# Performance work log

Hardware: AMD Instinct MI355X
Metric: run time of the kernel (lower is better)

The kernel has to match this reference:

```python
import jax, jax.numpy as jnp
import numpy as np

N_NODES = 100000
N_EDGES = 1600000
D_IN, D_HID, N_CLS = 256, 128, 47


def setup_inputs() -> dict:
    key = jax.random.key(0)
    k = jax.random.split(key, 5)
    x = jax.random.normal(k[0], (N_NODES, D_IN), dtype=jnp.float32)
    edge_index = jax.random.randint(k[1], (2, N_EDGES), 0, N_NODES, dtype=jnp.int64)
    W1 = jax.random.normal(k[2], (D_IN, D_HID), dtype=jnp.float32) * 0.05
    b1 = jnp.zeros((D_HID,), dtype=jnp.float32)
    W2 = jax.random.normal(k[3], (D_HID, N_CLS), dtype=jnp.float32) * 0.05
    b2 = jnp.zeros((N_CLS,), dtype=jnp.float32)
    return {"x": x, "edge_index": edge_index, "W1": W1, "b1": b1, "W2": W2, "b2": b2}


def _gcn_conv(x, W, b, src, dst, norm, n):
    # PyG GCNConv: linear transform, normalized scatter-add aggregation, bias after
    h = x @ W                                   # [N, D_out]
    msg = h[src] * norm[:, None]                # gather over edges [E', D_out]
    agg = jax.ops.segment_sum(msg, dst, num_segments=n)
    return agg + b


def reference(x, edge_index, W1, b1, W2, b2):
    n = x.shape[0]
    loop = jnp.arange(n, dtype=edge_index.dtype)
    src = jnp.concatenate([edge_index[0], loop])  # add self-loops
    dst = jnp.concatenate([edge_index[1], loop])
    # symmetric normalization D^-1/2 (A+I) D^-1/2 (degree = in-degree incl. self-loop)
    deg = jax.ops.segment_sum(jnp.ones_like(dst, dtype=x.dtype), dst, num_segments=n)
    dinv = jnp.where(deg > 0, jax.lax.rsqrt(deg), 0.0)
    norm = dinv[src] * dinv[dst]                 # [E']
    h1 = jax.nn.relu(_gcn_conv(x, W1, b1, src, dst, norm, n))
    # dropout with training=False is identity
    out = _gcn_conv(h1, W2, b2, src, dst, norm, n)
    return out
```

## Files before the change

### kernel.cpp

```cpp
#include <hip/hip_runtime.h>
#include <hip/hip_bf16.h>

#define DIN 256
#define DHID 128
#define NCLS 47
#define BSHIFT 9
#define BNODES 512
#define NPART 1024
#define BCAPS 9216
#define CHUNKE 1600

typedef __attribute__((ext_vector_type(8))) short short8;
typedef __attribute__((ext_vector_type(4))) float f32x4;

__device__ __forceinline__ short f2bf(float f) {
    __bf16 b = (__bf16)f;
    return __builtin_bit_cast(short, b);
}
__device__ __forceinline__ float bfu(unsigned int u) {
    return __uint_as_float(u << 16);
}
__device__ __forceinline__ float bfh(unsigned int u) {
    return __uint_as_float(u & 0xffff0000u);
}
__device__ __forceinline__ unsigned int pack2(float lo, float hi) {
    return (unsigned int)(unsigned short)f2bf(lo)
         | ((unsigned int)(unsigned short)f2bf(hi) << 16);
}
__device__ __forceinline__ void add8(float* a, uint4 v) {
    a[0] += bfu(v.x); a[1] += bfh(v.x);
    a[2] += bfu(v.y); a[3] += bfh(v.y);
    a[4] += bfu(v.z); a[5] += bfh(v.z);
    a[6] += bfu(v.w); a[7] += bfh(v.w);
}
__device__ __forceinline__ void fma8(float* a, uint4 v, float d) {
    a[0] += d * bfu(v.x); a[1] += d * bfh(v.x);
    a[2] += d * bfu(v.y); a[3] += d * bfh(v.y);
    a[4] += d * bfu(v.z); a[5] += d * bfh(v.z);
    a[6] += d * bfu(v.w); a[7] += d * bfh(v.w);
}

__global__ __launch_bounds__(256) void k_prep_hist(const float* __restrict__ W1,
                                                   const float* __restrict__ W2,
                                                   short* __restrict__ W1s,
                                                   short* __restrict__ W2s,
                                                   const int* __restrict__ dst,
                                                   int* __restrict__ ghist,
                                                   int E, int NB, int chunk) {
    __shared__ int lh[256];
    int blk = blockIdx.x, t = threadIdx.x;
    if (blk < 16) {
        int tid = blk * 256 + t;
        int frag = tid >> 6, lane = tid & 63;
        int kt = frag >> 3, nt = frag & 7;
        int quad = lane >> 4, col = lane & 15;
        #pragma unroll
        for (int j = 0; j < 8; ++j) {
            int k = kt * 32 + quad * 8 + j;
            W1s[(size_t)tid * 8 + j] = f2bf(W1[k * DHID + nt * 16 + col]);
        }
    } else if (blk < 20) {
        int tid = (blk - 16) * 256 + t;
        int frag = tid >> 6, lane = tid & 63;
        int kt = frag >> 2, nt = frag & 3;
        int quad = lane >> 4, col = lane & 15;
        int c = nt * 16 + col;
        #pragma unroll
        for (int j = 0; j < 8; ++j) {
            int k = kt * 32 + quad * 8 + j;
            float v = (c < NCLS) ? W2[k * NCLS + c] : 0.0f;
            W2s[(size_t)tid * 8 + j] = f2bf(v);
        }
    } else {
        int p = blk - 20;
        for (int i = t; i < NB; i += 256) lh[i] = 0;
        __syncthreads();
        int lo = p * chunk, hi = min(E, lo + chunk);
        for (int i = lo + t; i < hi; i += 256)
            atomicAdd(&lh[dst[i] >> BSHIFT], 1);
        __syncthreads();
        for (int i = t; i < NB; i += 256) ghist[(size_t)i * NPART + p] = lh[i];
    }
}

__global__ __launch_bounds__(256) void k_colscan(const int* __restrict__ ghist,
                                                 int* __restrict__ goff,
                                                 int* __restrict__ btot) {
    __shared__ int wsum[4];
    int b = blockIdx.x, t = threadIdx.x;
    int4 v = ((const int4*)(ghist + (size_t)b * NPART))[t];
    int s = v.x + v.y + v.z + v.w;
    int incl = s;
    int lane = t & 63, w = t >> 6;
    #pragma unroll
    for (int off = 1; off < 64; off <<= 1) {
        int u = __shfl_up(incl, off, 64);
        if (lane >= off) incl += u;
    }
    if (lane == 63) wsum[w] = incl;
    __syncthreads();
    int wadd = 0;
    for (int i = 0; i < w; ++i) wadd += wsum[i];
    int ex = wadd + incl - s;
    int4 o;
    o.x = ex; o.y = ex + v.x; o.z = o.y + v.y; o.w = o.z + v.z;
    ((int4*)(goff + (size_t)b * NPART))[t] = o;
    if (t == 255) btot[b] = wadd + incl;
}

__device__ __forceinline__ void scan_btot(const int* __restrict__ btot, int NB,
                                          int* lbase, int* wsum) {
    int t = threadIdx.x;
    int v = (t < NB) ? btot[t] : 0;
    int incl = v;
    int lane = t & 63, w = t >> 6;
    #pragma unroll
    for (int off = 1; off < 64; off <<= 1) {
        int u = __shfl_up(incl, off, 64);
        if (lane >= off) incl += u;
    }
    if (lane == 63) wsum[w] = incl;
    __syncthreads();
    int wadd = 0;
    for (int i = 0; i < w; ++i) wadd += wsum[i];
    lbase[t] = wadd + incl - v;
    __syncthreads();
}

__global__ __launch_bounds__(256) void k_scatter_gemm1(const int* __restrict__ src,
                                                       const int* __restrict__ dst,
                                                       const int* __restrict__ ghist,
                                                       const int* __restrict__ goff,
                                                       const int* __restrict__ btot,
                                                       unsigned int* __restrict__ bbuf,
                                                       int E, int NB, int chunk,
                                                       const float* __restrict__ x,
                                                       const short* __restrict__ W1s,
                                                       short* __restrict__ hb, int n) {
    __shared__ unsigned int stage[CHUNKE];
    __shared__ int sdest[CHUNKE];
    __shared__ int lcur[256];
    __shared__ int gdst[256];
    __shared__ int wsum[4];

    int blk = blockIdx.x, t = threadIdx.x;

    if (blk < NPART) {
        int p = blk;
        scan_btot(btot, NB, gdst, wsum);

        int mine = (t < NB) ? ghist[(size_t)t * NPART + p] : 0;
        int incl = mine;
        int lane = t & 63, w = t >> 6;
        #pragma unroll
        for (int off = 1; off < 64; off <<= 1) {
            int u = __shfl_up(incl, off, 64);
            if (lane >= off) incl += u;
        }
        if (lane == 63) wsum[w] = incl;
        __syncthreads();
        int wadd = 0;
        for (int i = 0; i < w; ++i) wadd += wsum[i];
        int ex = wadd + incl - mine;
        lcur[t] = ex;
        if (t < NB) gdst[t] += goff[(size_t)t * NPART + p] - ex;
        __syncthreads();

        int lo = p * chunk, hi = min(E, lo + chunk), cnt = hi - lo;
        for (int i = lo + t; i < hi; i += 256) {
            int d = dst[i];
            int b = d >> BSHIFT;
            int slot = atomicAdd(&lcur[b], 1);
            stage[slot] = (unsigned int)src[i] | ((unsigned int)(d & (BNODES - 1)) << 17);
            sdest[slot] = gdst[b] + slot;
        }
        __syncthreads();
        for (int i = t; i < cnt; i += 256)
            bbuf[sdest[i]] = stage[i];
    } else {
        int bid = blk - NPART;
        int wave = t >> 6, lane = t & 63;
        int quad = lane >> 4, lrow = lane & 15;
        long long rowbase = (long long)bid * 128 + wave * 32;

        f32x4 acc[2][8];
        #pragma unroll
        for (int rt = 0; rt < 2; ++rt)
            #pragma unroll
            for (int nt = 0; nt < 8; ++nt) acc[rt][nt] = (f32x4){0.f, 0.f, 0.f, 0.f};

        const short8* lf = (const short8*)W1s;

        #pragma unroll
        for (int kt = 0; kt < 8; ++kt) {
            int k0 = kt * 32 + quad * 8;
            short8 a[2];
            #pragma unroll
            for (int rt = 0; rt < 2; ++rt) {
                long long row = rowbase + rt * 16 + lrow;
                float4 v0 = {0.f,0.f,0.f,0.f}, v1 = {0.f,0.f,0.f,0.f};
                if (row < n) {
                    const float* xp = x + row * DIN + k0;
                    v0 = *(const float4*)xp;
                    v1 = *(const float4*)(xp + 4);
                }
                short8 av;
                av[0] = f2bf(v0.x); av[1] = f2bf(v0.y); av[2] = f2bf(v0.z); av[3] = f2bf(v0.w);
                av[4] = f2bf(v1.x); av[5] = f2bf(v1.y); av[6] = f2bf(v1.z); av[7] = f2bf(v1.w);
                a[rt] = av;
            }
            #pragma unroll
            for (int nt = 0; nt < 8; ++nt) {
                short8 b = lf[(kt * 8 + nt) * 64 + lane];
                acc[0][nt] = __builtin_amdgcn_mfma_f32_16x16x32_bf16(a[0], b, acc[0][nt], 0, 0, 0);
                acc[1][nt] = __builtin_amdgcn_mfma_f32_16x16x32_bf16(a[1], b, acc[1][nt], 0, 0, 0);
            }
        }
        #pragma unroll
        for (int rt = 0; rt < 2; ++rt)
            #pragma unroll
            for (int nt = 0; nt < 8; ++nt)
                #pragma unroll
                for (int r = 0; r < 4; ++r) {
                    long long row = rowbase + rt * 16 + quad * 4 + r;
                    if (row < n) hb[row * DHID + nt * 16 + lrow] = f2bf(acc[rt][nt][r]);
                }
    }
}

__global__ __launch_bounds__(512) void k_bsort(const int* __restrict__ btot,
                                               unsigned int* __restrict__ bbuf,
                                               int* __restrict__ degi,
                                               int* __restrict__ beg,
                                               float* __restrict__ dinv, int n, int NB) {
    __shared__ unsigned int stage[BCAPS];
    __shared__ int hist[BNODES];
    __shared__ int cur[BNODES];
    __shared__ int lbase[256];
    __shared__ int wsum[4];

    int b = blockIdx.x, t = threadIdx.x;

    if (t < 256) {
        int v = (t < NB) ? btot[t] : 0;
        int incl = v;
        int lane = t & 63, w = t >> 6;
        #pragma unroll
        for (int off = 1; off < 64; off <<= 1) {
            int u = __shfl_up(incl, off, 64);
            if (lane >= off) incl += u;
        }
        if (lane == 63) wsum[w] = incl;
        lbase[t] = v;
    }
    __syncthreads();
    if (t < 256) {
        int v = lbase[t];
        int incl = v;
        int lane = t & 63, w = t >> 6;
        #pragma unroll
        for (int off = 1; off < 64; off <<= 1) {
            int u = __shfl_up(incl, off, 64);
            if (lane >= off) incl += u;
        }
        int wadd = 0;
        for (int i = 0; i < w; ++i) wadd += wsum[i];
        lbase[t] = wadd + incl - v;
    }
    hist[t] = 0;
    __syncthreads();

    int cnt = min(btot[b], BCAPS);
    int gbase = lbase[b];
    int node0 = b << BSHIFT;

    for (int i = t; i < cnt; i += 512) {
        unsigned int p = bbuf[gbase + i];
        stage[i] = p;
        atomicAdd(&hist[p >> 17], 1);
    }
    __syncthreads();

    int v0 = 0, v1 = 0, ex = 0;
    if (t < 256) {
        v0 = hist[2 * t]; v1 = hist[2 * t + 1];
        int s = v0 + v1;
        int incl = s;
        int lane = t & 63, w = t >> 6;
        #pragma unroll
        for (int off = 1; off < 64; off <<= 1) {
            int u = __shfl_up(incl, off, 64);
            if (lane >= off) incl += u;
        }
        if (lane == 63) wsum[w] = incl;
        ex = incl - s;
    }
    __syncthreads();
    if (t < 256) {
        int lane = t & 63, w = t >> 6;
        (void)lane;
        int wadd = 0;
        for (int i = 0; i < w; ++i) wadd += wsum[i];
        ex += wadd;
        cur[2 * t] = ex;
        cur[2 * t + 1] = ex + v0;
        int nodeA = node0 + 2 * t, nodeB = node0 + 2 * t + 1;
        if (nodeA < n) {
            degi[nodeA] = v0;
            beg[nodeA]  = gbase + ex;
            dinv[nodeA] = rsqrtf((float)(v0 + 1));
        }
        if (nodeB < n) {
            degi[nodeB] = v1;
            beg[nodeB]  = gbase + ex + v0;
            dinv[nodeB] = rsqrtf((float)(v1 + 1));
        }
    }
    __syncthreads();

    for (int i = t; i < cnt; i += 512) {
        unsigned int p = stage[i];
        int slot = atomicAdd(&cur[p >> 17], 1);
        bbuf[gbase + slot] = p & 0x1FFFFu;
    }
}

__global__ __launch_bounds__(256) void k_gather1(const int* __restrict__ beg,
                          const int* __restrict__ degi,
                          const int* __restrict__ ssrc, const float* __restrict__ dinv,
                          const uint4* __restrict__ hb4, const float* __restrict__ b1,
                          uint4* __restrict__ h1u4, int n) {
    int node = blockIdx.x * 4 + (threadIdx.x >> 6);
    int t = threadIdx.x & 63;
    if (node >= n) return;
    int cnt = degi[node];
    int bg  = beg[node];
    int grp = t >> 4, sub = t & 15;

    float a[8] = {0.f,0.f,0.f,0.f,0.f,0.f,0.f,0.f};
    int k = 0;
    for (; k + 16 <= cnt; k += 16) {
        int s[4];
        #pragma unroll
        for (int q = 0; q < 4; ++q) s[q] = ssrc[bg + k + grp * 4 + q];
        float dv[4]; uint4 v[4];
        #pragma unroll
        for (int q = 0; q < 4; ++q) { dv[q] = dinv[s[q]]; v[q] = hb4[(size_t)s[q] * 16 + sub]; }
        #pragma unroll
        for (int q = 0; q < 4; ++q) fma8(a, v[q], dv[q]);
    }
    for (; k < cnt; k += 4) {
        int idx = k + grp;
        if (idx < cnt) {
            int s = ssrc[bg + idx];
            fma8(a, hb4[(size_t)s * 16 + sub], dinv[s]);
        }
    }

    #pragma unroll
    for (int j = 0; j < 8; ++j) {
        a[j] += __shfl_xor(a[j], 16);
        a[j] += __shfl_xor(a[j], 32);
    }

    if (grp == 0) {
        uint4 sv = hb4[(size_t)node * 16 + sub];
        float di = dinv[node], dd = di * di;
        float4 bA = ((const float4*)b1)[sub * 2];
        float4 bB = ((const float4*)b1)[sub * 2 + 1];
        float v0 = fmaxf(di * a[0] + dd * bfu(sv.x) + bA.x, 0.f);
        float v1 = fmaxf(di * a[1] + dd * bfh(sv.x) + bA.y, 0.f);
        float v2 = fmaxf(di * a[2] + dd * bfu(sv.y) + bA.z, 0.f);
        float v3 = fmaxf(di * a[3] + dd * bfh(sv.y) + bA.w, 0.f);
        float v4 = fmaxf(di * a[4] + dd * bfu(sv.z) + bB.x, 0.f);
        float v5 = fmaxf(di * a[5] + dd * bfh(sv.z) + bB.y, 0.f);
        float v6 = fmaxf(di * a[6] + dd * bfu(sv.w) + bB.z, 0.f);
        float v7 = fmaxf(di * a[7] + dd * bfh(sv.w) + bB.w, 0.f);
        uint4 o;
        o.x = pack2(v0, v1);
        o.y = pack2(v2, v3);
        o.z = pack2(v4, v5);
        o.w = pack2(v6, v7);
        h1u4[(size_t)node * 16 + sub] = o;
    }
}

__global__ __launch_bounds__(256) void k_gemm2_mfma(const short* __restrict__ h1b,
                                                    const short* __restrict__ W2s,
                                                    const float* __restrict__ dinv,
                                                    short* __restrict__ h2b, int n) {
    __shared__ short lw[8192];
    {
        const uint4* g = (const uint4*)W2s;
        uint4* l = (uint4*)lw;
        for (int i = threadIdx.x; i < 1024; i += 256) l[i] = g[i];
    }
    __syncthreads();

    int wave = threadIdx.x >> 6, lane = threadIdx.x & 63;
    int quad = lane >> 4, lrow = lane & 15;
    long long row0 = (long long)blockIdx.x * 64 + wave * 16;

    f32x4 acc[3];
    #pragma unroll
    for (int nt = 0; nt < 3; ++nt) acc[nt] = (f32x4){0.f, 0.f, 0.f, 0.f};

    const short8* lf = (const short8*)lw;

    #pragma unroll
    for (int kt = 0; kt < 4; ++kt) {
        long long row = row0 + lrow;
        short8 a = (short8){0,0,0,0,0,0,0,0};
        if (row < n) a = *(const short8*)(h1b + row * DHID + kt * 32 + quad * 8);
        #pragma unroll
        for (int nt = 0; nt < 3; ++nt)
            acc[nt] = __builtin_amdgcn_mfma_f32_16x16x32_bf16(a, lf[(kt * 4 + nt) * 64 + lane], acc[nt], 0, 0, 0);
    }
    float dvv[4];
    #pragma unroll
    for (int r = 0; r < 4; ++r) {
        long long row = row0 + quad * 4 + r;
        dvv[r] = (row < n) ? dinv[row] : 0.f;
    }
    #pragma unroll
    for (int nt = 0; nt < 3; ++nt)
        #pragma unroll
        for (int r = 0; r < 4; ++r) {
            long long row = row0 + quad * 4 + r;
            if (row < n) h2b[row * 48 + nt * 16 + lrow] = f2bf(acc[nt][r] * dvv[r]);
        }
}

__global__ __launch_bounds__(256) void k_gather2(const int* __restrict__ beg,
                          const int* __restrict__ degi,
                          const int* __restrict__ ssrc, const float* __restrict__ dinv,
                          const uint4* __restrict__ h2b6, const float* __restrict__ b2,
                          float* __restrict__ out, int n) {
    int node = blockIdx.x * 4 + (threadIdx.x >> 6);
    int t = threadIdx.x & 63;
    if (node >= n) return;
    int cnt = degi[node];
    int bg  = beg[node];
    int grp = t >> 3, sub = t & 7;

    float a[8] = {0.f,0.f,0.f,0.f,0.f,0.f,0.f,0.f};
    int k = 0;
    for (; k + 16 <= cnt; k += 16) {
        int s0 = ssrc[bg + k + grp], s1 = ssrc[bg + k + 8 + grp];
        if (sub < 6) {
            uint4 v0 = h2b6[(size_t)s0 * 6 + sub];
            uint4 v1 = h2b6[(size_t)s1 * 6 + sub];
            add8(a, v0); add8(a, v1);
        }
    }
    for (; k < cnt; k += 8) {
        int idx = k + grp;
        if (idx < cnt) {
            int s = ssrc[bg + idx];
            if (sub < 6) add8(a, h2b6[(size_t)s * 6 + sub]);
        }
    }
    if (grp == 0 && sub < 6) add8(a, h2b6[(size_t)node * 6 + sub]);

    #pragma unroll
    for (int j = 0; j < 8; ++j) {
        a[j] += __shfl_xor(a[j], 8);
        a[j] += __shfl_xor(a[j], 16);
        a[j] += __shfl_xor(a[j], 32);
    }

    if (grp == 0) {
        float di = dinv[node];
        #pragma unroll
        for (int j = 0; j < 8; ++j) {
            int c = sub * 8 + j;
            if (c < NCLS) out[(size_t)node * NCLS + c] = di * a[j] + b2[c];
        }
    }
}

extern "C" void kernel_launch(void* const* d_in, const int* in_sizes, int n_in,
                              void* d_out, int out_size, void* d_ws, size_t ws_size,
                              hipStream_t stream) {
    const float* x  = (const float*)d_in[0];
    const int*   ei = (const int*)d_in[1];
    const float* W1 = (const float*)d_in[2];
    const float* b1 = (const float*)d_in[3];
    const float* W2 = (const float*)d_in[4];
    const float* b2 = (const float*)d_in[5];

    const int n = in_sizes[0] / DIN;
    const int E = in_sizes[1] / 2;
    const int* src = ei;
    const int* dst = ei + E;
    float* out = (float*)d_out;

    const int NB = (n + BNODES - 1) >> BSHIFT;
    const int chunk = (E + NPART - 1) / NPART;

    char* w = (char*)d_ws;
    int*   ghist = (int*)w;                    w += (size_t)NB * NPART * 4;
    int*   goff  = (int*)w;                    w += (size_t)NB * NPART * 4;
    int*   btot  = (int*)w;                    w += ((size_t)256 * 4);
    int*   degi  = (int*)w;                    w += (size_t)n * 4;
    int*   beg   = (int*)w;                    w += (size_t)n * 4;
    float* dinv  = (float*)w;                  w += (size_t)n * 4;
    short* W1s   = (short*)w;                  w += (size_t)32768 * 2;
    short* W2s   = (short*)w;                  w += (size_t)8192 * 2;
    unsigned int* bbuf = (unsigned int*)w;     w += (size_t)E * 4;
    short* hb    = (short*)w;                  w += (size_t)n * DHID * 2;
    short* h1b   = (short*)w;                  w += (size_t)n * DHID * 2;
    short* h2b   = (short*)w;                  w += (size_t)n * 48 * 2;

    k_prep_hist<<<20 + NPART, 256, 0, stream>>>(W1, W2, W1s, W2s, dst, ghist, E, NB, chunk);
    k_colscan<<<NB, 256, 0, stream>>>(ghist, goff, btot);
    k_scatter_gemm1<<<NPART + (n + 127) / 128, 256, 0, stream>>>(src, dst, ghist, goff, btot,
                                                                 bbuf, E, NB, chunk,
                                                                 x, W1s, hb, n);
    k_bsort<<<NB, 512, 0, stream>>>(btot, bbuf, degi, beg, dinv, n, NB);
    k_gather1<<<(n + 3) / 4, 256, 0, stream>>>(beg, degi, (const int*)bbuf, dinv,
                                               (const uint4*)hb, b1,
                                               (uint4*)h1b, n);
    k_gemm2_mfma<<<(n + 63) / 64, 256, 0, stream>>>(h1b, W2s, dinv, h2b, n);
    k_gather2<<<(n + 3) / 4, 256, 0, stream>>>(beg, degi, (const int*)bbuf, dinv,
                                               (const uint4*)h2b, b2, out, n);
}
```

Before: 367.8 us.

## Move GEMM1 blocks from scatter kernel into bucket-sort kernel with LDS-staged weights

```diff
diff --git a/kernel.cpp b/kernel.cpp
--- a/kernel.cpp
+++ b/kernel.cpp
@@ -127,61 +127,166 @@
     __syncthreads();
 }
 
-__global__ __launch_bounds__(256) void k_scatter_gemm1(const int* __restrict__ src,
-                                                       const int* __restrict__ dst,
-                                                       const int* __restrict__ ghist,
-                                                       const int* __restrict__ goff,
-                                                       const int* __restrict__ btot,
-                                                       unsigned int* __restrict__ bbuf,
-                                                       int E, int NB, int chunk,
-                                                       const float* __restrict__ x,
-                                                       const short* __restrict__ W1s,
-                                                       short* __restrict__ hb, int n) {
+__global__ __launch_bounds__(256) void k_scatter(const int* __restrict__ src,
+                                                 const int* __restrict__ dst,
+                                                 const int* __restrict__ ghist,
+                                                 const int* __restrict__ goff,
+                                                 const int* __restrict__ btot,
+                                                 unsigned int* __restrict__ bbuf,
+                                                 int E, int NB, int chunk) {
     __shared__ unsigned int stage[CHUNKE];
     __shared__ int sdest[CHUNKE];
     __shared__ int lcur[256];
     __shared__ int gdst[256];
     __shared__ int wsum[4];
 
+    int p = blockIdx.x, t = threadIdx.x;
+    scan_btot(btot, NB, gdst, wsum);
+
+    int mine = (t < NB) ? ghist[(size_t)t * NPART + p] : 0;
+    int incl = mine;
+    int lane = t & 63, w = t >> 6;
+    #pragma unroll
+    for (int off = 1; off < 64; off <<= 1) {
+        int u = __shfl_up(incl, off, 64);
+        if (lane >= off) incl += u;
+    }
+    if (lane == 63) wsum[w] = incl;
+    __syncthreads();
+    int wadd = 0;
+    for (int i = 0; i < w; ++i) wadd += wsum[i];
+    int ex = wadd + incl - mine;
+    lcur[t] = ex;
+    if (t < NB) gdst[t] += goff[(size_t)t * NPART + p] - ex;
+    __syncthreads();
+
+    int lo = p * chunk, hi = min(E, lo + chunk), cnt = hi - lo;
+    for (int i = lo + t; i < hi; i += 256) {
+        int d = dst[i];
+        int b = d >> BSHIFT;
+        int slot = atomicAdd(&lcur[b], 1);
+        stage[slot] = (unsigned int)src[i] | ((unsigned int)(d & (BNODES - 1)) << 17);
+        sdest[slot] = gdst[b] + slot;
+    }
+    __syncthreads();
+    for (int i = t; i < cnt; i += 256)
+        bbuf[sdest[i]] = stage[i];
+}
+
+__global__ __launch_bounds__(512) void k_bsort_gemm1(const int* __restrict__ btot,
+                                                     unsigned int* __restrict__ bbuf,
+                                                     int* __restrict__ degi,
+                                                     int* __restrict__ beg,
+                                                     float* __restrict__ dinv,
+                                                     int n, int NB,
+                                                     const float* __restrict__ x,
+                                                     const short* __restrict__ W1s,
+                                                     short* __restrict__ hb) {
+    __shared__ __align__(16) char smem[65536];
     int blk = blockIdx.x, t = threadIdx.x;
 
-    if (blk < NPART) {
-        int p = blk;
-        scan_btot(btot, NB, gdst, wsum);
-
-        int mine = (t < NB) ? ghist[(size_t)t * NPART + p] : 0;
-        int incl = mine;
-        int lane = t & 63, w = t >> 6;
-        #pragma unroll
-        for (int off = 1; off < 64; off <<= 1) {
-            int u = __shfl_up(incl, off, 64);
-            if (lane >= off) incl += u;
-        }
-        if (lane == 63) wsum[w] = incl;
-        __syncthreads();
-        int wadd = 0;
-        for (int i = 0; i < w; ++i) wadd += wsum[i];
-        int ex = wadd + incl - mine;
-        lcur[t] = ex;
-        if (t < NB) gdst[t] += goff[(size_t)t * NPART + p] - ex;
-        __syncthreads();
-
-        int lo = p * chunk, hi = min(E, lo + chunk), cnt = hi - lo;
-        for (int i = lo + t; i < hi; i += 256) {
-            int d = dst[i];
-            int b = d >> BSHIFT;
-            int slot = atomicAdd(&lcur[b], 1);
-            stage[slot] = (unsigned int)src[i] | ((unsigned int)(d & (BNODES - 1)) << 17);
-            sdest[slot] = gdst[b] + slot;
-        }
-        __syncthreads();
-        for (int i = t; i < cnt; i += 256)
-            bbuf[sdest[i]] = stage[i];
+    if (blk < NB) {
+        unsigned int* stage = (unsigned int*)smem;
+        int* hist  = (int*)(smem + 36864);
+        int* cur   = (int*)(smem + 38912);
+        int* lbase = (int*)(smem + 40960);
+        int* wsum  = (int*)(smem + 41984);
+        int b = blk;
+
+        if (t < 256) {
+            int v = (t < NB) ? btot[t] : 0;
+            int incl = v;
+            int lane = t & 63, w = t >> 6;
+            #pragma unroll
+            for (int off = 1; off < 64; off <<= 1) {
+                int u = __shfl_up(incl, off, 64);
+                if (lane >= off) incl += u;
+            }
+            if (lane == 63) wsum[w] = incl;
+            lbase[t] = v;
+        }
+        __syncthreads();
+        if (t < 256) {
+            int v = lbase[t];
+            int incl = v;
+            int lane = t & 63, w = t >> 6;
+            #pragma unroll
+            for (int off = 1; off < 64; off <<= 1) {
+                int u = __shfl_up(incl, off, 64);
+                if (lane >= off) incl += u;
+            }
+            int wadd = 0;
+            for (int i = 0; i < w; ++i) wadd += wsum[i];
+            lbase[t] = wadd + incl - v;
+        }
+        hist[t] = 0;
+        __syncthreads();
+
+        int cnt = min(btot[b], BCAPS);
+        int gbase = lbase[b];
+        int node0 = b << BSHIFT;
+
+        for (int i = t; i < cnt; i += 512) {
+            unsigned int p = bbuf[gbase + i];
+            stage[i] = p;
+            atomicAdd(&hist[p >> 17], 1);
+        }
+        __syncthreads();
+
+        int v0 = 0, v1 = 0, ex = 0;
+        if (t < 256) {
+            v0 = hist[2 * t]; v1 = hist[2 * t + 1];
+            int s = v0 + v1;
+            int incl = s;
+            int lane = t & 63, w = t >> 6;
+            #pragma unroll
+            for (int off = 1; off < 64; off <<= 1) {
+                int u = __shfl_up(incl, off, 64);
+                if (lane >= off) incl += u;
+            }
+            if (lane == 63) wsum[w] = incl;
+            ex = incl - s;
+        }
+        __syncthreads();
+        if (t < 256) {
+            int w = t >> 6;
+            int wadd = 0;
+            for (int i = 0; i < w; ++i) wadd += wsum[i];
+            ex += wadd;
+            cur[2 * t] = ex;
+            cur[2 * t + 1] = ex + v0;
+            int nodeA = node0 + 2 * t, nodeB = node0 + 2 * t + 1;
+            if (nodeA < n) {
+                degi[nodeA] = v0;
+                beg[nodeA]  = gbase + ex;
+                dinv[nodeA] = rsqrtf((float)(v0 + 1));
+            }
+            if (nodeB < n) {
+                degi[nodeB] = v1;
+                beg[nodeB]  = gbase + ex + v0;
+                dinv[nodeB] = rsqrtf((float)(v1 + 1));
+            }
+        }
+        __syncthreads();
+
+        for (int i = t; i < cnt; i += 512) {
+            unsigned int p = stage[i];
+            int slot = atomicAdd(&cur[p >> 17], 1);
+            bbuf[gbase + slot] = p & 0x1FFFFu;
+        }
     } else {
-        int bid = blk - NPART;
+        short* lw = (short*)smem;
+        {
+            const uint4* g = (const uint4*)W1s;
+            uint4* l = (uint4*)lw;
+            for (int i = t; i < 4096; i += 512) l[i] = g[i];
+        }
+        __syncthreads();
+
+        int bid = blk - NB;
         int wave = t >> 6, lane = t & 63;
         int quad = lane >> 4, lrow = lane & 15;
-        long long rowbase = (long long)bid * 128 + wave * 32;
+        long long rowbase = (long long)bid * 256 + wave * 32;
 
         f32x4 acc[2][8];
         #pragma unroll
@@ -189,7 +294,7 @@
             #pragma unroll
             for (int nt = 0; nt < 8; ++nt) acc[rt][nt] = (f32x4){0.f, 0.f, 0.f, 0.f};
 
-        const short8* lf = (const short8*)W1s;
+        const short8* lf = (const short8*)lw;
 
         #pragma unroll
         for (int kt = 0; kt < 8; ++kt) {
@@ -225,103 +330,6 @@
                     long long row = rowbase + rt * 16 + quad * 4 + r;
                     if (row < n) hb[row * DHID + nt * 16 + lrow] = f2bf(acc[rt][nt][r]);
                 }
-    }
-}
-
-__global__ __launch_bounds__(512) void k_bsort(const int* __restrict__ btot,
-                                               unsigned int* __restrict__ bbuf,
-                                               int* __restrict__ degi,
-                                               int* __restrict__ beg,
-                                               float* __restrict__ dinv, int n, int NB) {
-    __shared__ unsigned int stage[BCAPS];
-    __shared__ int hist[BNODES];
-    __shared__ int cur[BNODES];
-    __shared__ int lbase[256];
-    __shared__ int wsum[4];
-
-    int b = blockIdx.x, t = threadIdx.x;
-
-    if (t < 256) {
-        int v = (t < NB) ? btot[t] : 0;
-        int incl = v;
-        int lane = t & 63, w = t >> 6;
-        #pragma unroll
-        for (int off = 1; off < 64; off <<= 1) {
-            int u = __shfl_up(incl, off, 64);
-            if (lane >= off) incl += u;
-        }
-        if (lane == 63) wsum[w] = incl;
-        lbase[t] = v;
-    }
-    __syncthreads();
-    if (t < 256) {
-        int v = lbase[t];
-        int incl = v;
-        int lane = t & 63, w = t >> 6;
-        #pragma unroll
-        for (int off = 1; off < 64; off <<= 1) {
-            int u = __shfl_up(incl, off, 64);
-            if (lane >= off) incl += u;
-        }
-        int wadd = 0;
-        for (int i = 0; i < w; ++i) wadd += wsum[i];
-        lbase[t] = wadd + incl - v;
-    }
-    hist[t] = 0;
-    __syncthreads();
-
-    int cnt = min(btot[b], BCAPS);
-    int gbase = lbase[b];
-    int node0 = b << BSHIFT;
-
-    for (int i = t; i < cnt; i += 512) {
-        unsigned int p = bbuf[gbase + i];
-        stage[i] = p;
-        atomicAdd(&hist[p >> 17], 1);
-    }
-    __syncthreads();
-
-    int v0 = 0, v1 = 0, ex = 0;
-    if (t < 256) {
-        v0 = hist[2 * t]; v1 = hist[2 * t + 1];
-        int s = v0 + v1;
-        int incl = s;
-        int lane = t & 63, w = t >> 6;
-        #pragma unroll
-        for (int off = 1; off < 64; off <<= 1) {
-            int u = __shfl_up(incl, off, 64);
-            if (lane >= off) incl += u;
-        }
-        if (lane == 63) wsum[w] = incl;
-        ex = incl - s;
-    }
-    __syncthreads();
-    if (t < 256) {
-        int lane = t & 63, w = t >> 6;
-        (void)lane;
-        int wadd = 0;
-        for (int i = 0; i < w; ++i) wadd += wsum[i];
-        ex += wadd;
-        cur[2 * t] = ex;
-        cur[2 * t + 1] = ex + v0;
-        int nodeA = node0 + 2 * t, nodeB = node0 + 2 * t + 1;
-        if (nodeA < n) {
-            degi[nodeA] = v0;
-            beg[nodeA]  = gbase + ex;
-            dinv[nodeA] = rsqrtf((float)(v0 + 1));
-        }
-        if (nodeB < n) {
-            degi[nodeB] = v1;
-            beg[nodeB]  = gbase + ex + v0;
-            dinv[nodeB] = rsqrtf((float)(v1 + 1));
-        }
-    }
-    __syncthreads();
-
-    for (int i = t; i < cnt; i += 512) {
-        unsigned int p = stage[i];
-        int slot = atomicAdd(&cur[p >> 17], 1);
-        bbuf[gbase + slot] = p & 0x1FFFFu;
     }
 }
 
@@ -514,10 +522,9 @@
 
     k_prep_hist<<<20 + NPART, 256, 0, stream>>>(W1, W2, W1s, W2s, dst, ghist, E, NB, chunk);
     k_colscan<<<NB, 256, 0, stream>>>(ghist, goff, btot);
-    k_scatter_gemm1<<<NPART + (n + 127) / 128, 256, 0, stream>>>(src, dst, ghist, goff, btot,
-                                                                 bbuf, E, NB, chunk,
-                                                                 x, W1s, hb, n);
-    k_bsort<<<NB, 512, 0, stream>>>(btot, bbuf, degi, beg, dinv, n, NB);
+    k_scatter<<<NPART, 256, 0, stream>>>(src, dst, ghist, goff, btot, bbuf, E, NB, chunk);
+    k_bsort_gemm1<<<NB + (n + 255) / 256, 512, 0, stream>>>(btot, bbuf, degi, beg, dinv,
+                                                            n, NB, x, W1s, hb);
     k_gather1<<<(n + 3) / 4, 256, 0, stream>>>(beg, degi, (const int*)bbuf, dinv,
                                                (const uint4*)hb, b1,
                                                (uint4*)h1b, n);
```

Measured after the change: 353.9 us. 1.04x faster.
